# Optimization experiments

Measured on AMD Instinct MI355X. Metric: run time of the kernel, lower is better.

## Reference

```python
import jax, jax.numpy as jnp
import numpy as np

B, S, H, HD, WIN, KS = 2, 2048, 8, 64, 64, 2048
D = H * HD          # slotsize = nheads * headsize = 512
SUB = 1 + 2 * WIN   # window length = 129
LN_EPS = 1e-3       # Keras LayerNormalization default epsilon


def setup_inputs() -> dict:
    key = jax.random.key(0)
    ks = jax.random.split(key, 5)
    s = 0.02
    return {
        "values": jax.random.normal(ks[0], (B, S, D), jnp.float32),
        "W_kqv": jax.random.normal(ks[1], (D, 3 * D), jnp.float32) * s,
        "b_kqv": jnp.zeros((3 * D,), jnp.float32),
        "ln_gamma": jnp.ones((D,), jnp.float32),
        "ln_beta": jnp.zeros((D,), jnp.float32),
        "W_kernel": jax.random.normal(ks[2], (D, KS), jnp.float32) * s,
        "b_kernel": jnp.zeros((KS,), jnp.float32),
        "W_proj": jax.random.normal(ks[3], (KS, D), jnp.float32) * s,
        "b_proj": jnp.zeros((D,), jnp.float32),
    }


def _layernorm(x, g, b):
    mu = jnp.mean(x, axis=-1, keepdims=True)
    var = jnp.var(x, axis=-1, keepdims=True)
    return (x - mu) * jax.lax.rsqrt(var + LN_EPS) * g + b


def reference(values, W_kqv, b_kqv, ln_gamma, ln_beta, W_kernel, b_kernel, W_proj, b_proj):
    # fused qkv projection: [B,S,3D]
    kqv = values @ W_kqv + b_kqv
    k, q, v = jnp.split(kqv, 3, axis=2)
    # shared layernorm applied to q and k (over full D)
    q = _layernorm(q, ln_gamma, ln_beta)
    k = _layernorm(k, ln_gamma, ln_beta)
    kh = k.reshape(B, S, H, HD)
    qh = q.reshape(B, S, H, HD)
    vh = v.reshape(B, S, H, HD)
    starts = jnp.clip(jnp.arange(S) - WIN, 0, S - SUB)
    idx = starts[:, None] + jnp.arange(SUB)          # [S, SUB]
    kw = kh[:, idx]                                  # [B,S,SUB,H,HD]
    vw = vh[:, idx]                                  # [B,S,SUB,H,HD]
    scores = jnp.einsum('bshd,bswhd->bshw', qh, kw) / np.float32(np.sqrt(HD))
    attn = jax.nn.softmax(scores, axis=-1)           # [B,S,H,SUB]
    ctx = jnp.einsum('bshw,bswhd->bshd', attn, vw).reshape(B, S, D)
    # residual MLP (dropout rate 0 -> identity)
    x = jax.nn.relu(ctx @ W_kernel + b_kernel)
    x = x @ W_proj + b_proj
    return x + v  # residual is the value projection, per the original code
```

## Files before the change

kernel.cpp:

```cpp
#include <hip/hip_runtime.h>
#include <hip/hip_bf16.h>

#define B_ 2
#define S_ 2048
#define H_ 8
#define HD_ 64
#define WIN_ 64
#define SUB_ 129
#define D_ 512
#define KS_ 2048
#define M_ 4096
#define LN_EPS 1e-3f

typedef unsigned short u16;
typedef short bf16x8 __attribute__((ext_vector_type(8)));
typedef float f32x4 __attribute__((ext_vector_type(4)));

__device__ inline u16 f2bf(float x) {
  unsigned int u = __float_as_uint(x);
  return (u16)((u + 0x7fffu + ((u >> 16) & 1u)) >> 16);
}
__device__ inline float bf2f(u16 u) {
  return __uint_as_float(((unsigned int)u) << 16);
}
__device__ inline float bf2f_lo(unsigned int u) { return __uint_as_float(u << 16); }
__device__ inline float bf2f_hi(unsigned int u) { return __uint_as_float(u & 0xffff0000u); }

__device__ inline void gll16(const u16* g, u16* l) {
  __builtin_amdgcn_global_load_lds(
      (const __attribute__((address_space(1))) void*)g,
      (__attribute__((address_space(3))) void*)l, 16, 0, 0);
}

template <int EPI>
__global__ __launch_bounds__(256) void mfma_gemm(
    const u16* __restrict__ A, const u16* __restrict__ Bt,
    const float* __restrict__ bias, u16* __restrict__ Cout, int K, int lda,
    int ldb, int ldc, int TN) {
  __shared__ __align__(16) u16 As[2][4096];
  __shared__ __align__(16) u16 Bs[2][4096];

  const int tid = threadIdx.x;
  const int wv = tid >> 6;
  const int ln = tid & 63;

  const int id = blockIdx.x;
  const int xcd = id & 7;
  const int sub = id >> 3;
  const int tn = sub % TN;
  const int msub = sub / TN;
  const int row0 = (xcd * 4 + msub) << 7;
  const int col0 = tn << 7;

  const int lrow = ln >> 2;
  const int lchunk = (ln & 3) ^ ((ln >> 3) & 3);
  const u16* ag = A + (size_t)(row0 + 32 * wv + lrow) * lda + lchunk * 8;
  const u16* bg = Bt + (size_t)(col0 + 32 * wv + lrow) * ldb + lchunk * 8;
  const int lbase = wv * 1024;

  const int quad = ln >> 4;
  const int l15 = ln & 15;
  const int pc = (quad ^ ((l15 >> 1) & 3)) << 4;
  const int wm = (wv & 1) << 6;
  const int wn = (wv >> 1) << 6;

  f32x4 acc[4][4];
#pragma unroll
  for (int i = 0; i < 4; ++i)
#pragma unroll
    for (int j = 0; j < 4; ++j) acc[i][j] = (f32x4){0.f, 0.f, 0.f, 0.f};

#define STAGE(buf, koff)                                            \
  do {                                                              \
    gll16(ag + (koff), &As[buf][lbase]);                            \
    gll16(ag + (koff) + 16 * (size_t)lda, &As[buf][lbase + 512]);   \
    gll16(bg + (koff), &Bs[buf][lbase]);                            \
    gll16(bg + (koff) + 16 * (size_t)ldb, &Bs[buf][lbase + 512]);   \
  } while (0)

  const int nk = K >> 5;
  STAGE(0, 0);

  for (int ki = 0; ki < nk; ++ki) {
    __syncthreads();
    if (ki + 1 < nk) STAGE((ki + 1) & 1, (ki + 1) << 5);

    const char* Ab = (const char*)As[ki & 1];
    const char* Bb = (const char*)Bs[ki & 1];
    bf16x8 af[4], bfv[4];
#pragma unroll
    for (int mi = 0; mi < 4; ++mi)
      af[mi] = *(const bf16x8*)(Ab + (wm + 16 * mi + l15) * 64 + pc);
#pragma unroll
    for (int ni = 0; ni < 4; ++ni)
      bfv[ni] = *(const bf16x8*)(Bb + (wn + 16 * ni + l15) * 64 + pc);
#pragma unroll
    for (int mi = 0; mi < 4; ++mi)
#pragma unroll
      for (int ni = 0; ni < 4; ++ni)
        acc[mi][ni] = __builtin_amdgcn_mfma_f32_16x16x32_bf16(
            bfv[ni], af[mi], acc[mi][ni], 0, 0, 0);
  }
#undef STAGE

  const int c00 = col0 + wn + (quad << 2);
  float4 bv[4];
#pragma unroll
  for (int ni = 0; ni < 4; ++ni) bv[ni] = *(const float4*)&bias[c00 + ni * 16];

#pragma unroll
  for (int mi = 0; mi < 4; ++mi) {
    const int row = row0 + wm + 16 * mi + l15;
#pragma unroll
    for (int ni = 0; ni < 4; ++ni) {
      float v0 = acc[mi][ni][0] + bv[ni].x;
      float v1 = acc[mi][ni][1] + bv[ni].y;
      float v2 = acc[mi][ni][2] + bv[ni].z;
      float v3 = acc[mi][ni][3] + bv[ni].w;
      if (EPI == 1) {
        v0 = fmaxf(v0, 0.f); v1 = fmaxf(v1, 0.f);
        v2 = fmaxf(v2, 0.f); v3 = fmaxf(v3, 0.f);
      }
      ushort4 o = {f2bf(v0), f2bf(v1), f2bf(v2), f2bf(v3)};
      *(ushort4*)&Cout[(size_t)row * ldc + c00 + ni * 16] = o;
    }
  }
}

__global__ __launch_bounds__(256) void mfma_gemm64(
    const u16* __restrict__ A, const u16* __restrict__ Bt,
    const float* __restrict__ bias, const u16* __restrict__ extra,
    float* __restrict__ Cout, int K, int lda, int ldb, int ldc, int eld,
    int TN, int MB) {
  __shared__ __align__(16) u16 As[2][2048];
  __shared__ __align__(16) u16 Bs[2][4096];

  const int tid = threadIdx.x;
  const int wv = tid >> 6;
  const int ln = tid & 63;

  const int id = blockIdx.x;
  const int xcd = id & 7;
  const int sub = id >> 3;
  const int tn = sub % TN;
  const int msub = sub / TN;
  const int row0 = (xcd * MB + msub) << 6;
  const int col0 = tn << 7;

  const int lrow = ln >> 2;
  const int lchunk = (ln & 3) ^ ((ln >> 3) & 3);
  const u16* ag = A + (size_t)(row0 + 16 * wv + lrow) * lda + lchunk * 8;
  const u16* bg = Bt + (size_t)(col0 + 32 * wv + lrow) * ldb + lchunk * 8;
  const int abase = wv * 512;
  const int bbase = wv * 1024;

  const int quad = ln >> 4;
  const int l15 = ln & 15;
  const int pc = (quad ^ ((l15 >> 1) & 3)) << 4;
  const int wn = wv << 5;

  f32x4 acc[4][2];
#pragma unroll
  for (int i = 0; i < 4; ++i)
#pragma unroll
    for (int j = 0; j < 2; ++j) acc[i][j] = (f32x4){0.f, 0.f, 0.f, 0.f};

#define STAGE64(buf, koff)                                          \
  do {                                                              \
    gll16(ag + (koff), &As[buf][abase]);                            \
    gll16(bg + (koff), &Bs[buf][bbase]);                            \
    gll16(bg + (koff) + 16 * (size_t)ldb, &Bs[buf][bbase + 512]);   \
  } while (0)

  const int nk = K >> 5;
  STAGE64(0, 0);

  for (int ki = 0; ki < nk; ++ki) {
    __syncthreads();
    if (ki + 1 < nk) STAGE64((ki + 1) & 1, (ki + 1) << 5);

    const char* Ab = (const char*)As[ki & 1];
    const char* Bb = (const char*)Bs[ki & 1];
    bf16x8 af[4], bfv[2];
#pragma unroll
    for (int mi = 0; mi < 4; ++mi)
      af[mi] = *(const bf16x8*)(Ab + (16 * mi + l15) * 64 + pc);
#pragma unroll
    for (int ni = 0; ni < 2; ++ni)
      bfv[ni] = *(const bf16x8*)(Bb + (wn + 16 * ni + l15) * 64 + pc);
#pragma unroll
    for (int mi = 0; mi < 4; ++mi)
#pragma unroll
      for (int ni = 0; ni < 2; ++ni)
        acc[mi][ni] = __builtin_amdgcn_mfma_f32_16x16x32_bf16(
            bfv[ni], af[mi], acc[mi][ni], 0, 0, 0);
  }
#undef STAGE64

  const int c00 = col0 + wn + (quad << 2);
  float4 bv[2];
#pragma unroll
  for (int ni = 0; ni < 2; ++ni) bv[ni] = *(const float4*)&bias[c00 + ni * 16];

#pragma unroll
  for (int mi = 0; mi < 4; ++mi) {
    const int row = row0 + 16 * mi + l15;
#pragma unroll
    for (int ni = 0; ni < 2; ++ni) {
      const int c = c00 + ni * 16;
      uint2 ex = *(const uint2*)&extra[(size_t)row * eld + c];
      float4 o;
      o.x = acc[mi][ni][0] + bv[ni].x + bf2f_lo(ex.x);
      o.y = acc[mi][ni][1] + bv[ni].y + bf2f_hi(ex.x);
      o.z = acc[mi][ni][2] + bv[ni].z + bf2f_lo(ex.y);
      o.w = acc[mi][ni][3] + bv[ni].w + bf2f_hi(ex.y);
      *(float4*)&Cout[(size_t)row * ldc + c] = o;
    }
  }
}

__global__ __launch_bounds__(256) void cvt_kernel(const float* __restrict__ in,
                                                  u16* __restrict__ out) {
  const int i = (blockIdx.x * 256 + threadIdx.x) * 8;
  float4 a = *(const float4*)&in[i];
  float4 b = *(const float4*)&in[i + 4];
  union { u16 u[8]; uint4 v; } pk;
  pk.u[0] = f2bf(a.x); pk.u[1] = f2bf(a.y); pk.u[2] = f2bf(a.z); pk.u[3] = f2bf(a.w);
  pk.u[4] = f2bf(b.x); pk.u[5] = f2bf(b.y); pk.u[6] = f2bf(b.z); pk.u[7] = f2bf(b.w);
  *(uint4*)&out[i] = pk.v;
}

__global__ __launch_bounds__(256) void cvtT_kernel(const float* __restrict__ W,
                                                   u16* __restrict__ Wt, int K,
                                                   int N) {
  __shared__ float t[32][33];
  const int n0 = blockIdx.x << 5;
  const int k0 = blockIdx.y << 5;
  const int r = threadIdx.x >> 3;
  const int c4 = (threadIdx.x & 7) << 2;
  float4 v = *(const float4*)&W[(size_t)(k0 + r) * N + n0 + c4];
  t[r][c4 + 0] = v.x; t[r][c4 + 1] = v.y; t[r][c4 + 2] = v.z; t[r][c4 + 3] = v.w;
  __syncthreads();
  ushort4 o;
  o.x = f2bf(t[c4 + 0][r]); o.y = f2bf(t[c4 + 1][r]);
  o.z = f2bf(t[c4 + 2][r]); o.w = f2bf(t[c4 + 3][r]);
  *(ushort4*)&Wt[(size_t)(n0 + r) * K + k0 + c4] = o;
}

__global__ __launch_bounds__(128) void ln_kernel(u16* __restrict__ kqv,
                                                 const float* __restrict__ gamma,
                                                 const float* __restrict__ beta) {
  const int row = blockIdx.x;
  const int bs = row >> 1;
  const int which = row & 1;
  u16* p = kqv + (size_t)bs * 1536 + (which ? 512 : 0);
  const int tid = threadIdx.x;
  const int c = tid << 2;

  uint2 raw = *(uint2*)&p[c];
  float x0 = bf2f_lo(raw.x), x1 = bf2f_hi(raw.x);
  float x2 = bf2f_lo(raw.y), x3 = bf2f_hi(raw.y);
  float s = x0 + x1 + x2 + x3;
  float ss = x0 * x0 + x1 * x1 + x2 * x2 + x3 * x3;

#pragma unroll
  for (int off = 32; off > 0; off >>= 1) {
    s += __shfl_down(s, off);
    ss += __shfl_down(ss, off);
  }
  __shared__ float red[4];
  if ((tid & 63) == 0) {
    red[(tid >> 6) * 2 + 0] = s;
    red[(tid >> 6) * 2 + 1] = ss;
  }
  __syncthreads();
  const float tot = red[0] + red[2];
  const float tots = red[1] + red[3];
  const float mean = tot * (1.f / 512.f);
  const float var = tots * (1.f / 512.f) - mean * mean;
  const float rstd = rsqrtf(var + LN_EPS);

  float4 g = *(const float4*)&gamma[c];
  float4 bb = *(const float4*)&beta[c];
  union { u16 u[4]; uint2 v; } o;
  o.u[0] = f2bf((x0 - mean) * rstd * g.x + bb.x);
  o.u[1] = f2bf((x1 - mean) * rstd * g.y + bb.y);
  o.u[2] = f2bf((x2 - mean) * rstd * g.z + bb.z);
  o.u[3] = f2bf((x3 - mean) * rstd * g.w + bb.w);
  *(uint2*)&p[c] = o.v;
}

__global__ __launch_bounds__(256) void attn_kernel(const u16* __restrict__ kqv,
                                                   u16* __restrict__ ctx) {
  __shared__ __align__(16) u16 Ks[192 * 64];
  __shared__ __align__(16) u16 Vt[64 * 192];
  __shared__ __align__(16) u16 Ps[4 * 16 * 192];

  const int bid = blockIdx.x;
  const int tile = bid & 31;
  const int h = (bid >> 5) & 7;
  const int b = bid >> 8;
  const int t0 = tile << 6;

  int g0 = t0 - WIN_;
  if (g0 < 0) g0 = 0;
  if (g0 > S_ - SUB_) g0 = S_ - SUB_;

  const int tid = threadIdx.x;
  const size_t rowb = (size_t)(b * S_);

#pragma unroll
  for (int it = 0; it < 6; ++it) {
    const int item = tid + it * 256;
    const int key = item >> 3, c = item & 7;
    const int phys = c ^ (key & 7);
    uint4 v = *(const uint4*)&kqv[(rowb + g0 + key) * 1536 + h * 64 + c * 8];
    *(uint4*)&Ks[key * 64 + phys * 8] = v;
  }
#pragma unroll
  for (int it = 0; it < 2; ++it) {
    const int item = tid + it * 256;
    const int qq = item >> 3, c = item & 7;
    const int phys = c ^ (qq & 7);
    uint4 v = *(const uint4*)&kqv[(rowb + t0 + qq) * 1536 + 512 + h * 64 + c * 8];
    *(uint4*)&Ps[qq * 64 + phys * 8] = v;
  }
#pragma unroll
  for (int it = 0; it < 12; ++it) {
    const int item = tid + it * 256;
    const int dg = item / 192;
    const int key = item - dg * 192;
    uint2 v = *(const uint2*)&kqv[(rowb + g0 + key) * 1536 + 1024 + h * 64 + dg * 4];
    const int c = key >> 3;
    u16 e[4] = {(u16)(v.x & 0xffff), (u16)(v.x >> 16),
                (u16)(v.y & 0xffff), (u16)(v.y >> 16)};
#pragma unroll
    for (int j = 0; j < 4; ++j) {
      const int d = dg * 4 + j;
      const int phys = (c & 24) | ((c ^ d) & 7);
      Vt[d * 192 + phys * 8 + (key & 7)] = e[j];
    }
  }
  __syncthreads();

  const int wv = tid >> 6;
  const int ln = tid & 63;
  const int quad = ln >> 4;
  const int l15 = ln & 15;
  const int l7 = l15 & 7;
  const int qbase = wv << 4;

  bf16x8 qf[2];
#pragma unroll
  for (int ks = 0; ks < 2; ++ks) {
    const int phys = (ks * 4 + quad) ^ l7;
    qf[ks] = *(const bf16x8*)&Ps[(qbase + l15) * 64 + phys * 8];
  }

  f32x4 sacc[12];
#pragma unroll
  for (int nt = 0; nt < 12; ++nt) sacc[nt] = (f32x4){0.f, 0.f, 0.f, 0.f};
#pragma unroll
  for (int ks = 0; ks < 2; ++ks) {
    const int phys = (ks * 4 + quad) ^ l7;
#pragma unroll
    for (int nt = 0; nt < 12; ++nt) {
      bf16x8 kf = *(const bf16x8*)&Ks[(nt * 16 + l15) * 64 + phys * 8];
      sacc[nt] = __builtin_amdgcn_mfma_f32_16x16x32_bf16(qf[ks], kf, sacc[nt], 0, 0, 0);
    }
  }

  int off[4];
#pragma unroll
  for (int r = 0; r < 4; ++r) {
    const int qg = t0 + qbase + quad * 4 + r;
    int st = qg - WIN_;
    if (st < 0) st = 0;
    if (st > S_ - SUB_) st = S_ - SUB_;
    off[r] = st - g0;
  }

  float rmax[4] = {-1e30f, -1e30f, -1e30f, -1e30f};
#pragma unroll
  for (int nt = 0; nt < 12; ++nt) {
    const int n = nt * 16 + l15;
#pragma unroll
    for (int r = 0; r < 4; ++r) {
      const bool valid = (n >= off[r]) && (n < off[r] + SUB_);
      const float v = valid ? sacc[nt][r] * 0.125f : -1e30f;
      sacc[nt][r] = v;
      rmax[r] = fmaxf(rmax[r], v);
    }
  }
#pragma unroll
  for (int m = 1; m < 16; m <<= 1)
#pragma unroll
    for (int r = 0; r < 4; ++r) rmax[r] = fmaxf(rmax[r], __shfl_xor(rmax[r], m));

  float rsum[4] = {0.f, 0.f, 0.f, 0.f};
#pragma unroll
  for (int nt = 0; nt < 12; ++nt) {
#pragma unroll
    for (int r = 0; r < 4; ++r) {
      const float e = __expf(sacc[nt][r] - rmax[r]);
      sacc[nt][r] = e;
      rsum[r] += e;
    }
  }
#pragma unroll
  for (int m = 1; m < 16; m <<= 1)
#pragma unroll
    for (int r = 0; r < 4; ++r) rsum[r] += __shfl_xor(rsum[r], m);
  float inv[4];
#pragma unroll
  for (int r = 0; r < 4; ++r) inv[r] = 1.f / rsum[r];

  __syncthreads();

  u16* psw = &Ps[wv * 16 * 192];
#pragma unroll
  for (int nt = 0; nt < 12; ++nt) {
    const int n = nt * 16 + l15;
    const int c = n >> 3;
#pragma unroll
    for (int r = 0; r < 4; ++r) {
      const int m = quad * 4 + r;
      const int phys = (c & 24) | ((c ^ m) & 7);
      psw[m * 192 + phys * 8 + (n & 7)] = f2bf(sacc[nt][r]);
    }
  }
  __syncthreads();

  f32x4 oacc[4];
#pragma unroll
  for (int nt = 0; nt < 4; ++nt) oacc[nt] = (f32x4){0.f, 0.f, 0.f, 0.f};
#pragma unroll
  for (int ks = 0; ks < 6; ++ks) {
    const int c = ks * 4 + quad;
    const int phys = (c & 24) | ((c ^ l7) & 7);
    bf16x8 pf = *(const bf16x8*)&psw[l15 * 192 + phys * 8];
#pragma unroll
    for (int nt = 0; nt < 4; ++nt) {
      bf16x8 vf = *(const bf16x8*)&Vt[(nt * 16 + l15) * 192 + phys * 8];
      oacc[nt] = __builtin_amdgcn_mfma_f32_16x16x32_bf16(pf, vf, oacc[nt], 0, 0, 0);
    }
  }

#pragma unroll
  for (int nt = 0; nt < 4; ++nt) {
#pragma unroll
    for (int r = 0; r < 4; ++r) {
      const int row = t0 + qbase + quad * 4 + r;
      const int col = h * 64 + nt * 16 + l15;
      ctx[(rowb + row) * D_ + col] = f2bf(oacc[nt][r] * inv[r]);
    }
  }
}

extern "C" void kernel_launch(void* const* d_in, const int* in_sizes, int n_in,
                              void* d_out, int out_size, void* d_ws,
                              size_t ws_size, hipStream_t stream) {
  (void)in_sizes; (void)n_in; (void)out_size; (void)ws_size;
  const float* values   = (const float*)d_in[0];
  const float* W_kqv    = (const float*)d_in[1];
  const float* b_kqv    = (const float*)d_in[2];
  const float* ln_gamma = (const float*)d_in[3];
  const float* ln_beta  = (const float*)d_in[4];
  const float* W_kernel = (const float*)d_in[5];
  const float* b_kernel = (const float*)d_in[6];
  const float* W_proj   = (const float*)d_in[7];
  const float* b_proj   = (const float*)d_in[8];
  float* out = (float*)d_out;

  u16* kqv     = (u16*)d_ws;
  u16* vals_bf = kqv + (size_t)M_ * 1536;
  u16* ctx_bf  = vals_bf + (size_t)M_ * 512;
  u16* x_bf    = ctx_bf + (size_t)M_ * 512;
  u16* wkqv_t  = x_bf + (size_t)M_ * 2048;
  u16* wker_t  = wkqv_t + (size_t)1536 * 512;
  u16* wproj_t = wker_t + (size_t)2048 * 512;

  cvt_kernel<<<(M_ * 512) / 2048, 256, 0, stream>>>(values, vals_bf);
  cvtT_kernel<<<dim3(1536 / 32, 512 / 32), 256, 0, stream>>>(W_kqv, wkqv_t, 512, 1536);
  cvtT_kernel<<<dim3(2048 / 32, 512 / 32), 256, 0, stream>>>(W_kernel, wker_t, 512, 2048);
  cvtT_kernel<<<dim3(512 / 32, 2048 / 32), 256, 0, stream>>>(W_proj, wproj_t, 2048, 512);

  mfma_gemm<3><<<384, 256, 0, stream>>>(
      vals_bf, wkqv_t, b_kqv, kqv, 512, 512, 512, 1536, 12);

  ln_kernel<<<2 * M_, 128, 0, stream>>>(kqv, ln_gamma, ln_beta);

  attn_kernel<<<B_ * H_ * (S_ / 64), 256, 0, stream>>>(kqv, ctx_bf);

  mfma_gemm<1><<<512, 256, 0, stream>>>(
      ctx_bf, wker_t, b_kernel, x_bf, 512, 512, 512, KS_, 16);

  mfma_gemm64<<<256, 256, 0, stream>>>(
      x_bf, wproj_t, b_proj, kqv + 1024, out, KS_, KS_, KS_, D_, 1536, 4, 8);
}
```

Measured before the change: 172.7 us.

## Double GEMM K-tile to 64 with 8-way swizzle and fuse conversion kernels

After: 160.8 us. -6.9%, faster.

```diff
diff --git a/kernel.cpp b/kernel.cpp
--- a/kernel.cpp
+++ b/kernel.cpp
@@ -20,9 +20,6 @@
   unsigned int u = __float_as_uint(x);
   return (u16)((u + 0x7fffu + ((u >> 16) & 1u)) >> 16);
 }
-__device__ inline float bf2f(u16 u) {
-  return __uint_as_float(((unsigned int)u) << 16);
-}
 __device__ inline float bf2f_lo(unsigned int u) { return __uint_as_float(u << 16); }
 __device__ inline float bf2f_hi(unsigned int u) { return __uint_as_float(u & 0xffff0000u); }
 
@@ -37,8 +34,8 @@
     const u16* __restrict__ A, const u16* __restrict__ Bt,
     const float* __restrict__ bias, u16* __restrict__ Cout, int K, int lda,
     int ldb, int ldc, int TN) {
-  __shared__ __align__(16) u16 As[2][4096];
-  __shared__ __align__(16) u16 Bs[2][4096];
+  __shared__ __align__(16) u16 As[2][8192];
+  __shared__ __align__(16) u16 Bs[2][8192];
 
   const int tid = threadIdx.x;
   const int wv = tid >> 6;
@@ -52,15 +49,15 @@
   const int row0 = (xcd * 4 + msub) << 7;
   const int col0 = tn << 7;
 
-  const int lrow = ln >> 2;
-  const int lchunk = (ln & 3) ^ ((ln >> 3) & 3);
+  const int lrow = ln >> 3;
+  const int lchunk = (ln & 7) ^ lrow;
   const u16* ag = A + (size_t)(row0 + 32 * wv + lrow) * lda + lchunk * 8;
   const u16* bg = Bt + (size_t)(col0 + 32 * wv + lrow) * ldb + lchunk * 8;
-  const int lbase = wv * 1024;
+  const int lbase = 32 * wv * 64;
 
   const int quad = ln >> 4;
   const int l15 = ln & 15;
-  const int pc = (quad ^ ((l15 >> 1) & 3)) << 4;
+  const int r7 = l15 & 7;
   const int wm = (wv & 1) << 6;
   const int wn = (wv >> 1) << 6;
 
@@ -72,34 +69,46 @@
 
 #define STAGE(buf, koff)                                            \
   do {                                                              \
-    gll16(ag + (koff), &As[buf][lbase]);                            \
-    gll16(ag + (koff) + 16 * (size_t)lda, &As[buf][lbase + 512]);   \
-    gll16(bg + (koff), &Bs[buf][lbase]);                            \
-    gll16(bg + (koff) + 16 * (size_t)ldb, &Bs[buf][lbase + 512]);   \
+    const u16* a0 = ag + (koff);                                    \
+    const u16* b0 = bg + (koff);                                    \
+    u16* la = &As[buf][lbase];                                      \
+    u16* lb = &Bs[buf][lbase];                                      \
+    gll16(a0, la);                                                  \
+    gll16(a0 + 8 * (size_t)lda, la + 512);                          \
+    gll16(a0 + 16 * (size_t)lda, la + 1024);                        \
+    gll16(a0 + 24 * (size_t)lda, la + 1536);                        \
+    gll16(b0, lb);                                                  \
+    gll16(b0 + 8 * (size_t)ldb, lb + 512);                          \
+    gll16(b0 + 16 * (size_t)ldb, lb + 1024);                        \
+    gll16(b0 + 24 * (size_t)ldb, lb + 1536);                        \
   } while (0)
 
-  const int nk = K >> 5;
+  const int nk = K >> 6;
   STAGE(0, 0);
 
   for (int ki = 0; ki < nk; ++ki) {
     __syncthreads();
-    if (ki + 1 < nk) STAGE((ki + 1) & 1, (ki + 1) << 5);
+    if (ki + 1 < nk) STAGE((ki + 1) & 1, (ki + 1) << 6);
 
     const char* Ab = (const char*)As[ki & 1];
     const char* Bb = (const char*)Bs[ki & 1];
-    bf16x8 af[4], bfv[4];
-#pragma unroll
-    for (int mi = 0; mi < 4; ++mi)
-      af[mi] = *(const bf16x8*)(Ab + (wm + 16 * mi + l15) * 64 + pc);
-#pragma unroll
-    for (int ni = 0; ni < 4; ++ni)
-      bfv[ni] = *(const bf16x8*)(Bb + (wn + 16 * ni + l15) * 64 + pc);
-#pragma unroll
-    for (int mi = 0; mi < 4; ++mi)
+#pragma unroll
+    for (int ks = 0; ks < 2; ++ks) {
+      const int pc = ((quad + 4 * ks) ^ r7) << 4;
+      bf16x8 af[4], bfv[4];
+#pragma unroll
+      for (int mi = 0; mi < 4; ++mi)
+        af[mi] = *(const bf16x8*)(Ab + (wm + 16 * mi + l15) * 128 + pc);
 #pragma unroll
       for (int ni = 0; ni < 4; ++ni)
-        acc[mi][ni] = __builtin_amdgcn_mfma_f32_16x16x32_bf16(
-            bfv[ni], af[mi], acc[mi][ni], 0, 0, 0);
+        bfv[ni] = *(const bf16x8*)(Bb + (wn + 16 * ni + l15) * 128 + pc);
+#pragma unroll
+      for (int mi = 0; mi < 4; ++mi)
+#pragma unroll
+        for (int ni = 0; ni < 4; ++ni)
+          acc[mi][ni] = __builtin_amdgcn_mfma_f32_16x16x32_bf16(
+              bfv[ni], af[mi], acc[mi][ni], 0, 0, 0);
+    }
   }
 #undef STAGE
 
@@ -132,8 +141,8 @@
     const float* __restrict__ bias, const u16* __restrict__ extra,
     float* __restrict__ Cout, int K, int lda, int ldb, int ldc, int eld,
     int TN, int MB) {
-  __shared__ __align__(16) u16 As[2][2048];
-  __shared__ __align__(16) u16 Bs[2][4096];
+  __shared__ __align__(16) u16 As[2][4096];
+  __shared__ __align__(16) u16 Bs[2][8192];
 
   const int tid = threadIdx.x;
   const int wv = tid >> 6;
@@ -147,16 +156,14 @@
   const int row0 = (xcd * MB + msub) << 6;
   const int col0 = tn << 7;
 
-  const int lrow = ln >> 2;
-  const int lchunk = (ln & 3) ^ ((ln >> 3) & 3);
+  const int lrow = ln >> 3;
+  const int lchunk = (ln & 7) ^ lrow;
   const u16* ag = A + (size_t)(row0 + 16 * wv + lrow) * lda + lchunk * 8;
   const u16* bg = Bt + (size_t)(col0 + 32 * wv + lrow) * ldb + lchunk * 8;
-  const int abase = wv * 512;
-  const int bbase = wv * 1024;
 
   const int quad = ln >> 4;
   const int l15 = ln & 15;
-  const int pc = (quad ^ ((l15 >> 1) & 3)) << 4;
+  const int r7 = l15 & 7;
   const int wn = wv << 5;
 
   f32x4 acc[4][2];
@@ -167,33 +174,44 @@
 
 #define STAGE64(buf, koff)                                          \
   do {                                                              \
-    gll16(ag + (koff), &As[buf][abase]);                            \
-    gll16(bg + (koff), &Bs[buf][bbase]);                            \
-    gll16(bg + (koff) + 16 * (size_t)ldb, &Bs[buf][bbase + 512]);   \
+    const u16* a0 = ag + (koff);                                    \
+    const u16* b0 = bg + (koff);                                    \
+    u16* la = &As[buf][wv * 1024];                                  \
+    u16* lb = &Bs[buf][wv * 2048];                                  \
+    gll16(a0, la);                                                  \
+    gll16(a0 + 8 * (size_t)lda, la + 512);                          \
+    gll16(b0, lb);                                                  \
+    gll16(b0 + 8 * (size_t)ldb, lb + 512);                          \
+    gll16(b0 + 16 * (size_t)ldb, lb + 1024);                        \
+    gll16(b0 + 24 * (size_t)ldb, lb + 1536);                        \
   } while (0)
 
-  const int nk = K >> 5;
+  const int nk = K >> 6;
   STAGE64(0, 0);
 
   for (int ki = 0; ki < nk; ++ki) {
     __syncthreads();
-    if (ki + 1 < nk) STAGE64((ki + 1) & 1, (ki + 1) << 5);
+    if (ki + 1 < nk) STAGE64((ki + 1) & 1, (ki + 1) << 6);
 
     const char* Ab = (const char*)As[ki & 1];
     const char* Bb = (const char*)Bs[ki & 1];
-    bf16x8 af[4], bfv[2];
-#pragma unroll
-    for (int mi = 0; mi < 4; ++mi)
-      af[mi] = *(const bf16x8*)(Ab + (16 * mi + l15) * 64 + pc);
-#pragma unroll
-    for (int ni = 0; ni < 2; ++ni)
-      bfv[ni] = *(const bf16x8*)(Bb + (wn + 16 * ni + l15) * 64 + pc);
-#pragma unroll
-    for (int mi = 0; mi < 4; ++mi)
+#pragma unroll
+    for (int ks = 0; ks < 2; ++ks) {
+      const int pc = ((quad + 4 * ks) ^ r7) << 4;
+      bf16x8 af[4], bfv[2];
+#pragma unroll
+      for (int mi = 0; mi < 4; ++mi)
+        af[mi] = *(const bf16x8*)(Ab + (16 * mi + l15) * 128 + pc);
 #pragma unroll
       for (int ni = 0; ni < 2; ++ni)
-        acc[mi][ni] = __builtin_amdgcn_mfma_f32_16x16x32_bf16(
-            bfv[ni], af[mi], acc[mi][ni], 0, 0, 0);
+        bfv[ni] = *(const bf16x8*)(Bb + (wn + 16 * ni + l15) * 128 + pc);
+#pragma unroll
+      for (int mi = 0; mi < 4; ++mi)
+#pragma unroll
+        for (int ni = 0; ni < 2; ++ni)
+          acc[mi][ni] = __builtin_amdgcn_mfma_f32_16x16x32_bf16(
+              bfv[ni], af[mi], acc[mi][ni], 0, 0, 0);
+    }
   }
 #undef STAGE64
 
@@ -219,23 +237,29 @@
   }
 }
 
-__global__ __launch_bounds__(256) void cvt_kernel(const float* __restrict__ in,
-                                                  u16* __restrict__ out) {
-  const int i = (blockIdx.x * 256 + threadIdx.x) * 8;
-  float4 a = *(const float4*)&in[i];
-  float4 b = *(const float4*)&in[i + 4];
-  union { u16 u[8]; uint4 v; } pk;
-  pk.u[0] = f2bf(a.x); pk.u[1] = f2bf(a.y); pk.u[2] = f2bf(a.z); pk.u[3] = f2bf(a.w);
-  pk.u[4] = f2bf(b.x); pk.u[5] = f2bf(b.y); pk.u[6] = f2bf(b.z); pk.u[7] = f2bf(b.w);
-  *(uint4*)&out[i] = pk.v;
-}
-
-__global__ __launch_bounds__(256) void cvtT_kernel(const float* __restrict__ W,
-                                                   u16* __restrict__ Wt, int K,
-                                                   int N) {
+__global__ __launch_bounds__(256) void fused_cvt(
+    const float* __restrict__ values, u16* __restrict__ vals_bf,
+    const float* __restrict__ Wkqv, u16* __restrict__ wkqv_t,
+    const float* __restrict__ Wker, u16* __restrict__ wker_t,
+    const float* __restrict__ Wproj, u16* __restrict__ wproj_t) {
   __shared__ float t[32][33];
-  const int n0 = blockIdx.x << 5;
-  const int k0 = blockIdx.y << 5;
+  const int id = blockIdx.x;
+  if (id < 1024) {
+    const int i = (id * 256 + threadIdx.x) * 8;
+    float4 a = *(const float4*)&values[i];
+    float4 b = *(const float4*)&values[i + 4];
+    union { u16 u[8]; uint4 v; } pk;
+    pk.u[0] = f2bf(a.x); pk.u[1] = f2bf(a.y); pk.u[2] = f2bf(a.z); pk.u[3] = f2bf(a.w);
+    pk.u[4] = f2bf(b.x); pk.u[5] = f2bf(b.y); pk.u[6] = f2bf(b.z); pk.u[7] = f2bf(b.w);
+    *(uint4*)&vals_bf[i] = pk.v;
+    return;
+  }
+  const float* W; u16* Wt; int K, N, nx, lin;
+  if (id < 1792)      { lin = id - 1024; W = Wkqv;  Wt = wkqv_t;  K = 512;  N = 1536; nx = 48; }
+  else if (id < 2816) { lin = id - 1792; W = Wker;  Wt = wker_t;  K = 512;  N = 2048; nx = 64; }
+  else                { lin = id - 2816; W = Wproj; Wt = wproj_t; K = 2048; N = 512;  nx = 16; }
+  const int n0 = (lin % nx) << 5;
+  const int k0 = (lin / nx) << 5;
   const int r = threadIdx.x >> 3;
   const int c4 = (threadIdx.x & 7) << 2;
   float4 v = *(const float4*)&W[(size_t)(k0 + r) * N + n0 + c4];
@@ -480,10 +504,8 @@
   u16* wker_t  = wkqv_t + (size_t)1536 * 512;
   u16* wproj_t = wker_t + (size_t)2048 * 512;
 
-  cvt_kernel<<<(M_ * 512) / 2048, 256, 0, stream>>>(values, vals_bf);
-  cvtT_kernel<<<dim3(1536 / 32, 512 / 32), 256, 0, stream>>>(W_kqv, wkqv_t, 512, 1536);
-  cvtT_kernel<<<dim3(2048 / 32, 512 / 32), 256, 0, stream>>>(W_kernel, wker_t, 512, 2048);
-  cvtT_kernel<<<dim3(512 / 32, 2048 / 32), 256, 0, stream>>>(W_proj, wproj_t, 2048, 512);
+  fused_cvt<<<3840, 256, 0, stream>>>(values, vals_bf, W_kqv, wkqv_t,
+                                      W_kernel, wker_t, W_proj, wproj_t);
 
   mfma_gemm<3><<<384, 256, 0, stream>>>(
       vals_bf, wkqv_t, b_kqv, kqv, 512, 512, 512, 1536, 12);
```
